# Performance work log

Hardware: AMD Instinct MI355X
Metric: run time of the kernel (lower is better)

## Reference

```python
import jax, jax.numpy as jnp
import numpy as np
import math

B, Q, K, D = 16, 2048, 2048, 128


def setup_inputs() -> dict:
    key = jax.random.key(0)
    kq, kk, kv, kl = jax.random.split(key, 4)
    queries = jax.random.normal(kq, (B, Q, D), dtype=jnp.float32)
    keys = jax.random.normal(kk, (B, K, D), dtype=jnp.float32)
    values = jax.random.normal(kv, (B, K, D), dtype=jnp.float32)
    valid_lens = jax.random.randint(kl, (B,), 1, K + 1, dtype=jnp.int32)
    return {"queries": queries, "keys": keys, "values": values, "valid_lens": valid_lens}


def reference(queries, keys, values, valid_lens):
    d = queries.shape[-1]
    # scores = bmm(Q, K^T) // sqrt(d)  -- source uses floor-division, kept faithfully
    scores = jnp.floor(jnp.einsum('bqd,bkd->bqk', queries, keys) / math.sqrt(d))
    # masked_softmax: positions >= valid_len[b] get -1e6 before softmax
    mask = jnp.arange(keys.shape[1]) < valid_lens[:, None, None]  # [B,1,K]
    scores = jnp.where(mask, scores, -1e6)
    attn = jax.nn.softmax(scores, axis=-1)
    # dropout in eval mode = identity
    return jnp.einsum('bqk,bkv->bqv', attn, values)
```

## Files before the change

kernel.cpp:

```cpp
#include <hip/hip_runtime.h>
#include <cmath>

typedef __attribute__((ext_vector_type(4))) float f32x4;
typedef __attribute__((ext_vector_type(8))) _Float16 f16x8;
typedef __attribute__((ext_vector_type(4))) _Float16 f16x4;

#define B_SZ 16
#define Q_SZ 2048
#define K_SZ 2048
#define D_SZ 128
#define BQ   64
#define BKT  64
#define PST  72
#define SCL  0.08838834764831845f

#define GLDS16(g, s) __builtin_amdgcn_global_load_lds(                      \
    (const __attribute__((address_space(1))) unsigned int*)(g),             \
    (__attribute__((address_space(3))) unsigned int*)(s), 16, 0, 0)

__global__ __launch_bounds__(256) void prep_all(
    const float* __restrict__ K, const float* __restrict__ V,
    _Float16* __restrict__ Khi, _Float16* __restrict__ Klo,
    _Float16* __restrict__ Vt)
{
  __shared__ _Float16 tmp[64][136];
  const int tid = threadIdx.x;
  if (blockIdx.x < 2048) {
    const int gid = blockIdx.x * 256 + tid;
    const int r = gid >> 4;
    const int g = gid & 15;
    const float* src = K + (size_t)r * D_SZ + g * 8;
    f16x8 hi, lo;
#pragma unroll
    for (int i = 0; i < 8; ++i) {
      float x = src[i];
      _Float16 h = (_Float16)x;
      hi[i] = h;
      lo[i] = (_Float16)((x - (float)h) * 2048.0f);
    }
    const size_t o = (size_t)r * D_SZ + ((g ^ (r & 7)) * 8);
    *(f16x8*)(Khi + o) = hi;
    *(f16x8*)(Klo + o) = lo;
  } else {
    const int vb = blockIdx.x - 2048;
    const int b = vb >> 5;
    const int k0 = (vb & 31) * 64;
    const float* Vb = V + ((size_t)b * K_SZ + k0) * D_SZ;
#pragma unroll
    for (int j = 0; j < 8; ++j) {
      const int e = j * 1024 + tid * 4;
      const int k = e >> 7, d = e & 127;
      const f32x4 v = *(const f32x4*)(Vb + (size_t)k * D_SZ + d);
      f16x4 h;
#pragma unroll
      for (int i = 0; i < 4; ++i) h[i] = (_Float16)v[i];
      *(f16x4*)&tmp[k][d] = h;
    }
    __syncthreads();
#pragma unroll
    for (int i = 0; i < 4; ++i) {
      const int id = i * 256 + tid;
      const int gk = id >> 7, d = id & 127;
      f16x8 o;
#pragma unroll
      for (int jj = 0; jj < 8; ++jj) o[jj] = tmp[gk * 8 + jj][d];
      _Float16* dst = Vt + ((size_t)b * D_SZ + d) * K_SZ + k0 + ((gk ^ (d & 7)) * 8);
      *(f16x8*)dst = o;
    }
  }
}

__global__ __launch_bounds__(256, 2) void attn(
    const float* __restrict__ Qm, const _Float16* __restrict__ KhiG,
    const _Float16* __restrict__ KloG, const _Float16* __restrict__ VtG,
    const int* __restrict__ vlp, float* __restrict__ Om,
    float* __restrict__ P1, float* __restrict__ L0, float* __restrict__ L1,
    unsigned* __restrict__ cnt, const int split)
{
  __shared__ __align__(16) char sm[49152 + 64 * PST * 2];
  char* smKhi_c = sm;
  char* smKlo_c = sm + 16384;
  char* smVt_c  = sm + 32768;
  _Float16* smKhi = (_Float16*)smKhi_c;
  _Float16* smKlo = (_Float16*)smKlo_c;
  _Float16* smVt  = (_Float16*)smVt_c;
  _Float16* smP   = (_Float16*)(sm + 49152);
  __shared__ int s_task;
  __shared__ float Ls[2][2][32];

  const int tid  = threadIdx.x;
  const int wave = tid >> 6;
  const int lane = tid & 63;
  const int ln   = lane & 15;
  const int quad = lane >> 4;
  const int qh   = wave >> 1;
  const int kh   = wave & 1;

  for (;;) {
    int t;
    if (split) {
      if (tid == 0) s_task = (int)atomicAdd(cnt, 1u);
      __syncthreads();
      t = s_task;
      __syncthreads();
      if (t >= 1024) return;
    } else {
      t = blockIdx.x;
    }

    int half = 0, b, qt;
    if (split) { half = (t >= 512); const int u = t & 511; b = u >> 5; qt = u & 31; }
    else       { b = t >> 5; qt = t & 31; }
    const int q0     = qt * BQ;
    const int valid  = vlp[b];
    const int kstart = half * 1024;
    const int kend   = split ? min(valid, kstart + 1024) : valid;
    if (kend <= kstart) { if (!split) return; continue; }
    const int ntiles = (kend - kstart + BKT - 1) / BKT;

    const float* Qb    = Qm + (size_t)b * Q_SZ * D_SZ;
    const char*  gKhiB = (const char*)KhiG + (size_t)b * K_SZ * 256;
    const char*  gKloB = (const char*)KloG + (size_t)b * K_SZ * 256;
    const char*  gVtB  = (const char*)VtG  + (size_t)b * D_SZ * (K_SZ * 2);

    f16x8 qhi[2][4], qlo[2][4];
#pragma unroll
    for (int mt = 0; mt < 2; ++mt) {
      const int qrow = q0 + qh * 32 + mt * 16 + ln;
      const float* srcb = Qb + (size_t)qrow * D_SZ + quad * 8;
#pragma unroll
      for (int c = 0; c < 4; ++c) {
#pragma unroll
        for (int j = 0; j < 8; ++j) {
          float x = srcb[c * 32 + j];
          _Float16 h = (_Float16)x;
          qhi[mt][c][j] = h;
          qlo[mt][c][j] = (_Float16)((x - (float)h) * 2048.0f);
        }
      }
    }

    const f32x4 vzero = {0.f, 0.f, 0.f, 0.f};
    f32x4 accO[2][4];
    float lsum[8];
#pragma unroll
    for (int mt = 0; mt < 2; ++mt)
#pragma unroll
      for (int nb = 0; nb < 4; ++nb) accO[mt][nb] = vzero;
#pragma unroll
    for (int i = 0; i < 8; ++i) lsum[i] = 0.0f;

    for (int kt = 0; kt < ntiles; ++kt) {
      const int k0g = kstart + kt * BKT;

      {
        const char* gh = gKhiB + (size_t)k0g * 256;
        const char* gl = gKloB + (size_t)k0g * 256;
#pragma unroll
        for (int i = 0; i < 4; ++i) {
          const int off = (wave * 4 + i) * 1024;
          GLDS16(gh + off + lane * 16, smKhi_c + off);
          GLDS16(gl + off + lane * 16, smKlo_c + off);
        }
#pragma unroll
        for (int i = 0; i < 4; ++i) {
          const int off = (wave * 4 + i) * 1024;
          const int a = off + lane * 16;
          const int d = a >> 7, win = a & 127;
          GLDS16(gVtB + (size_t)d * (K_SZ * 2) + (size_t)k0g * 2 + win, smVt_c + off);
        }
      }
      __syncthreads();

      f32x4 accM[2][2], accC[2][2];
#pragma unroll
      for (int mt = 0; mt < 2; ++mt)
#pragma unroll
        for (int nb = 0; nb < 2; ++nb) { accM[mt][nb] = vzero; accC[mt][nb] = vzero; }
#pragma unroll
      for (int nb = 0; nb < 2; ++nb) {
        const int row = kh * 32 + nb * 16 + ln;
        const _Float16* bh_base = smKhi + row * 128;
        const _Float16* bl_base = smKlo + row * 128;
#pragma unroll
        for (int c = 0; c < 4; ++c) {
          const int pg = (((c * 4 + quad) ^ (ln & 7)) * 8);
          const f16x8 bh = *(const f16x8*)(bh_base + pg);
          const f16x8 bl = *(const f16x8*)(bl_base + pg);
#pragma unroll
          for (int mt = 0; mt < 2; ++mt) {
            accM[mt][nb] = __builtin_amdgcn_mfma_f32_16x16x32_f16(qhi[mt][c], bh, accM[mt][nb], 0, 0, 0);
            accC[mt][nb] = __builtin_amdgcn_mfma_f32_16x16x32_f16(qhi[mt][c], bl, accC[mt][nb], 0, 0, 0);
            accC[mt][nb] = __builtin_amdgcn_mfma_f32_16x16x32_f16(qlo[mt][c], bh, accC[mt][nb], 0, 0, 0);
          }
        }
      }

#pragma unroll
      for (int nb = 0; nb < 2; ++nb) {
        const int  key = k0g + kh * 32 + nb * 16 + ln;
        const bool ok  = key < valid;
#pragma unroll
        for (int mt = 0; mt < 2; ++mt) {
#pragma unroll
          for (int r = 0; r < 4; ++r) {
            const float s = accM[mt][nb][r] + accC[mt][nb][r] * (1.0f / 2048.0f);
            const float e = ok ? __expf(floorf(s * SCL)) : 0.0f;
            lsum[mt * 4 + r] += e;
            smP[(qh * 32 + mt * 16 + quad * 4 + r) * PST + kh * 32 + nb * 16 + ln] = (_Float16)e;
          }
        }
      }
      __syncthreads();

#pragma unroll
      for (int c = 0; c < 2; ++c) {
        f16x8 af[2];
#pragma unroll
        for (int mt = 0; mt < 2; ++mt)
          af[mt] = *(const f16x8*)(smP + (qh * 32 + mt * 16 + ln) * PST + c * 32 + quad * 8);
#pragma unroll
        for (int nb = 0; nb < 4; ++nb) {
          const int drow = kh * 64 + nb * 16 + ln;
          const int pg = (((c * 4 + quad) ^ (ln & 7)) * 8);
          const f16x8 bf = *(const f16x8*)(smVt + drow * 64 + pg);
#pragma unroll
          for (int mt = 0; mt < 2; ++mt)
            accO[mt][nb] = __builtin_amdgcn_mfma_f32_16x16x32_f16(af[mt], bf, accO[mt][nb], 0, 0, 0);
        }
      }
      __syncthreads();
    }

#pragma unroll
    for (int i = 0; i < 8; ++i) {
      float v = lsum[i];
      v += __shfl_xor(v, 1, 64);
      v += __shfl_xor(v, 2, 64);
      v += __shfl_xor(v, 4, 64);
      v += __shfl_xor(v, 8, 64);
      lsum[i] = v;
    }

    if (split) {
      float* Lh = half ? L1 : L0;
      if (ln == 0) {
#pragma unroll
        for (int mt = 0; mt < 2; ++mt)
#pragma unroll
          for (int r = 0; r < 4; ++r)
            atomicAdd(Lh + b * Q_SZ + q0 + qh * 32 + mt * 16 + quad * 4 + r, lsum[mt * 4 + r]);
      }
      float* dst = (half ? P1 : Om) + ((size_t)(b * Q_SZ + q0)) * D_SZ;
#pragma unroll
      for (int mt = 0; mt < 2; ++mt)
#pragma unroll
        for (int nb = 0; nb < 4; ++nb)
#pragma unroll
          for (int r = 0; r < 4; ++r)
            dst[(size_t)(qh * 32 + mt * 16 + quad * 4 + r) * D_SZ + kh * 64 + nb * 16 + ln] =
                accO[mt][nb][r];
    } else {
      if (ln == 0) {
#pragma unroll
        for (int mt = 0; mt < 2; ++mt)
#pragma unroll
          for (int r = 0; r < 4; ++r)
            Ls[qh][kh][mt * 16 + quad * 4 + r] = lsum[mt * 4 + r];
      }
      __syncthreads();
      float* Ob = Om + (size_t)b * Q_SZ * D_SZ;
#pragma unroll
      for (int mt = 0; mt < 2; ++mt) {
#pragma unroll
        for (int r = 0; r < 4; ++r) {
          const int rr = mt * 16 + quad * 4 + r;
          const float inv = 1.0f / (Ls[qh][0][rr] + Ls[qh][1][rr]);
#pragma unroll
          for (int nb = 0; nb < 4; ++nb)
            Ob[(size_t)(q0 + qh * 32 + rr) * D_SZ + kh * 64 + nb * 16 + ln] =
                accO[mt][nb][r] * inv;
        }
      }
    }
    if (!split) return;
  }
}

__global__ __launch_bounds__(256) void finalize(
    float* __restrict__ Om, const float* __restrict__ P1,
    const float* __restrict__ L0, const float* __restrict__ L1,
    const int* __restrict__ vlp)
{
  const int idx = blockIdx.x * 256 + threadIdx.x;
  const size_t e = (size_t)idx * 4;
  const int row = (int)(e >> 7);
  const int b = row >> 11;
  const int valid = vlp[b];
  f32x4 o = *(const f32x4*)(Om + e);
  float l = L0[row];
  if (valid > 1024) {
    const f32x4 p = *(const f32x4*)(P1 + e);
    o += p;
    l += L1[row];
  }
  const float inv = 1.0f / l;
  o *= inv;
  *(f32x4*)(Om + e) = o;
}

extern "C" void kernel_launch(void* const* d_in, const int* in_sizes, int n_in,
                              void* d_out, int out_size, void* d_ws, size_t ws_size,
                              hipStream_t stream) {
  const float* Qm = (const float*)d_in[0];
  const float* Km = (const float*)d_in[1];
  const float* Vm = (const float*)d_in[2];
  const int*   vl = (const int*)d_in[3];
  float*       Om = (float*)d_out;

  const size_t elems = (size_t)B_SZ * K_SZ * D_SZ;
  const size_t PREP  = 3 * elems * sizeof(_Float16);
  const size_t HDR   = 262400;
  const size_t P1SZ  = elems * sizeof(float);
  char* W = (char*)d_ws;

  if (ws_size >= HDR + PREP + P1SZ) {
    unsigned* cnt = (unsigned*)W;
    float*    L0  = (float*)(W + 256);
    float*    L1  = (float*)(W + 256 + 131072);
    _Float16* Khi = (_Float16*)(W + HDR);
    _Float16* Klo = Khi + elems;
    _Float16* Vt  = Klo + elems;
    float*    P1  = (float*)(W + HDR + PREP);
    hipMemsetAsync(d_ws, 0, HDR, stream);
    prep_all<<<2560, 256, 0, stream>>>(Km, Vm, Khi, Klo, Vt);
    attn<<<512, 256, 0, stream>>>(Qm, Khi, Klo, Vt, vl, Om, P1, L0, L1, cnt, 1);
    finalize<<<4096, 256, 0, stream>>>(Om, P1, L0, L1, vl);
  } else {
    _Float16* Khi = (_Float16*)W;
    _Float16* Klo = Khi + elems;
    _Float16* Vt  = Klo + elems;
    prep_all<<<2560, 256, 0, stream>>>(Km, Vm, Khi, Klo, Vt);
    attn<<<512, 256, 0, stream>>>(Qm, Khi, Klo, Vt, vl, Om,
                                  nullptr, nullptr, nullptr, nullptr, 0);
  }
}
```

Before: 168.8 us.

## Alias P buffer onto K tiles, raise occupancy, add per-XCD work queues

Places the softmax probability tile in the same shared memory as the K hi tile, with an extra barrier after the QK MFMAs, so LDS per block shrinks enough to allow 3 blocks per CU. The grid grows to 768 blocks to match. The single global atomic task counter becomes eight queues. Each block reads its XCC id from a hardware register and pulls work for batches tied to that XCD first, so K/V data should stay in that XCD's L2; it steals from other queues when its own is empty. Q loads are also vectorized to float4. The costs are an extra barrier per tile, a tighter register budget from the higher occupancy bound, and dependence on the XCC_ID register encoding.

```diff
diff --git a/kernel.cpp b/kernel.cpp
--- a/kernel.cpp
+++ b/kernel.cpp
@@ -70,22 +70,22 @@
   }
 }
 
-__global__ __launch_bounds__(256, 2) void attn(
+__global__ __launch_bounds__(256, 3) void attn(
     const float* __restrict__ Qm, const _Float16* __restrict__ KhiG,
     const _Float16* __restrict__ KloG, const _Float16* __restrict__ VtG,
     const int* __restrict__ vlp, float* __restrict__ Om,
     float* __restrict__ P1, float* __restrict__ L0, float* __restrict__ L1,
     unsigned* __restrict__ cnt, const int split)
 {
-  __shared__ __align__(16) char sm[49152 + 64 * PST * 2];
+  __shared__ __align__(16) char sm[49152];
   char* smKhi_c = sm;
   char* smKlo_c = sm + 16384;
   char* smVt_c  = sm + 32768;
   _Float16* smKhi = (_Float16*)smKhi_c;
   _Float16* smKlo = (_Float16*)smKlo_c;
   _Float16* smVt  = (_Float16*)smVt_c;
-  _Float16* smP   = (_Float16*)(sm + 49152);
-  __shared__ int s_task;
+  _Float16* smP   = (_Float16*)sm;
+  __shared__ int s_task, s_q;
   __shared__ float Ls[2][2][32];
 
   const int tid  = threadIdx.x;
@@ -96,21 +96,33 @@
   const int qh   = wave >> 1;
   const int kh   = wave & 1;
 
+  int home = 0, off = 0;
+  if (split) home = __builtin_amdgcn_s_getreg((3 << 11) | 20) & 7;
+
   for (;;) {
-    int t;
+    int t, qq;
     if (split) {
-      if (tid == 0) s_task = (int)atomicAdd(cnt, 1u);
-      __syncthreads();
-      t = s_task;
-      __syncthreads();
-      if (t >= 1024) return;
+      if (tid == 0) {
+        int tt = -1, qv = 0;
+        while (off < 8) {
+          qv = (home + off) & 7;
+          const unsigned v = atomicAdd(&cnt[qv], 1u);
+          if (v < 128u) { tt = (int)v; break; }
+          ++off;
+        }
+        s_task = tt; s_q = qv;
+      }
+      __syncthreads();
+      t = s_task; qq = s_q;
+      __syncthreads();
+      if (t < 0) return;
     } else {
-      t = blockIdx.x;
-    }
-
-    int half = 0, b, qt;
-    if (split) { half = (t >= 512); const int u = t & 511; b = u >> 5; qt = u & 31; }
-    else       { b = t >> 5; qt = t & 31; }
+      t = blockIdx.x; qq = 0;
+    }
+
+    int half, b, qt;
+    if (split) { half = (t >= 64); const int u = t & 63; b = (qq & 7) + 8 * (u >> 5); qt = u & 31; }
+    else       { half = 0; b = t >> 5; qt = t & 31; }
     const int q0     = qt * BQ;
     const int valid  = vlp[b];
     const int kstart = half * 1024;
@@ -130,12 +142,16 @@
       const float* srcb = Qb + (size_t)qrow * D_SZ + quad * 8;
 #pragma unroll
       for (int c = 0; c < 4; ++c) {
-#pragma unroll
-        for (int j = 0; j < 8; ++j) {
-          float x = srcb[c * 32 + j];
-          _Float16 h = (_Float16)x;
-          qhi[mt][c][j] = h;
-          qlo[mt][c][j] = (_Float16)((x - (float)h) * 2048.0f);
+        const f32x4 x0 = *(const f32x4*)(srcb + c * 32);
+        const f32x4 x1 = *(const f32x4*)(srcb + c * 32 + 4);
+#pragma unroll
+        for (int j = 0; j < 4; ++j) {
+          const _Float16 h0 = (_Float16)x0[j];
+          qhi[mt][c][j] = h0;
+          qlo[mt][c][j] = (_Float16)((x0[j] - (float)h0) * 2048.0f);
+          const _Float16 h1 = (_Float16)x1[j];
+          qhi[mt][c][j + 4] = h1;
+          qlo[mt][c][j + 4] = (_Float16)((x1[j] - (float)h1) * 2048.0f);
         }
       }
     }
@@ -158,16 +174,16 @@
         const char* gl = gKloB + (size_t)k0g * 256;
 #pragma unroll
         for (int i = 0; i < 4; ++i) {
-          const int off = (wave * 4 + i) * 1024;
-          GLDS16(gh + off + lane * 16, smKhi_c + off);
-          GLDS16(gl + off + lane * 16, smKlo_c + off);
+          const int o = (wave * 4 + i) * 1024;
+          GLDS16(gh + o + lane * 16, smKhi_c + o);
+          GLDS16(gl + o + lane * 16, smKlo_c + o);
         }
 #pragma unroll
         for (int i = 0; i < 4; ++i) {
-          const int off = (wave * 4 + i) * 1024;
-          const int a = off + lane * 16;
+          const int o = (wave * 4 + i) * 1024;
+          const int a = o + lane * 16;
           const int d = a >> 7, win = a & 127;
-          GLDS16(gVtB + (size_t)d * (K_SZ * 2) + (size_t)k0g * 2 + win, smVt_c + off);
+          GLDS16(gVtB + (size_t)d * (K_SZ * 2) + (size_t)k0g * 2 + win, smVt_c + o);
         }
       }
       __syncthreads();
@@ -195,6 +211,7 @@
           }
         }
       }
+      __syncthreads();
 
 #pragma unroll
       for (int nb = 0; nb < 2; ++nb) {
@@ -334,7 +351,7 @@
     float*    P1  = (float*)(W + HDR + PREP);
     hipMemsetAsync(d_ws, 0, HDR, stream);
     prep_all<<<2560, 256, 0, stream>>>(Km, Vm, Khi, Klo, Vt);
-    attn<<<512, 256, 0, stream>>>(Qm, Khi, Klo, Vt, vl, Om, P1, L0, L1, cnt, 1);
+    attn<<<768, 256, 0, stream>>>(Qm, Khi, Klo, Vt, vl, Om, P1, L0, L1, cnt, 1);
     finalize<<<4096, 256, 0, stream>>>(Om, P1, L0, L1, vl);
   } else {
     _Float16* Khi = (_Float16*)W;
```

Result: slower. 212.6 us (+26.0%).
